# Kernel optimization log

Hardware: AMD Instinct MI355X
Metric: run time of the kernel (lower is better)

## Reference

```python
import jax, jax.numpy as jnp
import numpy as np

B, CIN, COUT, N, K = 8, 128, 128, 2000, 16
IN_EPS = 1e-3   # InstanceNorm2d eps in module
BN_EPS = 1e-5   # BatchNorm2d default eps


def conv1x1(x, w, b):
    # x: [B,C,H,W], w: [O,C], b: [O]
    return jnp.einsum('bchw,oc->bohw', x, w) + b[None, :, None, None]


def setup_inputs() -> dict:
    key = jax.random.key(0)
    ks = jax.random.split(key, 12)
    s = 0.05
    return {
        'x_row':   jax.random.normal(ks[0], (B, COUT, N, 1), jnp.float32),
        'x_local': jax.random.normal(ks[1], (B, CIN, N, K), jnp.float32),
        'w0': jax.random.normal(ks[2], (COUT, CIN), jnp.float32) * s,
        'b0': jax.random.normal(ks[3], (COUT,), jnp.float32) * s,
        'bn_g': jnp.ones((COUT,), jnp.float32),
        'bn_b': jnp.zeros((COUT,), jnp.float32),
        'wq': jax.random.normal(ks[4], (COUT, COUT), jnp.float32) * s,
        'bq': jax.random.normal(ks[5], (COUT,), jnp.float32) * s,
        'wk': jax.random.normal(ks[6], (COUT, COUT), jnp.float32) * s,
        'bk': jax.random.normal(ks[7], (COUT,), jnp.float32) * s,
        'wv': jax.random.normal(ks[8], (COUT, COUT), jnp.float32) * s,
        'bv': jax.random.normal(ks[9], (COUT,), jnp.float32) * s,
        'gamma1': jnp.ones((1,), jnp.float32),
    }


def reference(x_row, x_local, w0, b0, bn_g, bn_b, wq, bq, wk, bk, wv, bv, gamma1):
    # att1: Conv1x1 -> InstanceNorm2d(eps=1e-3, no affine) -> BatchNorm2d (train-mode batch stats) -> ReLU
    h = conv1x1(x_local, w0, b0)                       # [B,C,N,K]
    mu = jnp.mean(h, axis=(2, 3), keepdims=True)
    var = jnp.var(h, axis=(2, 3), keepdims=True)
    h = (h - mu) * jax.lax.rsqrt(var + IN_EPS)
    bmu = jnp.mean(h, axis=(0, 2, 3), keepdims=True)
    bvar = jnp.var(h, axis=(0, 2, 3), keepdims=True)
    h = (h - bmu) * jax.lax.rsqrt(bvar + BN_EPS)
    h = h * bn_g[None, :, None, None] + bn_b[None, :, None, None]
    h = jax.nn.relu(h)

    q = conv1x1(h, wq, bq)
    k = conv1x1(h, wk, bk)
    v = conv1x1(h, wv, bv)
    att = jax.nn.softmax(q * k, axis=3)                # softmax over neighbor axis
    out_local = jnp.sum(att * v, axis=3, keepdims=True)  # [B,C,N,1]
    return x_row + gamma1 * out_local
```

## Files before the change

### kernel.cpp

```cpp
#include <hip/hip_runtime.h>
#include <math.h>

#define NB 8
#define NC 128
#define NPOS 2000
#define NK 32000
#define IN_EPS 1e-3f
#define BN_EPS 1e-5f

typedef short bf16x8 __attribute__((ext_vector_type(8)));
typedef float f32x4 __attribute__((ext_vector_type(4)));
typedef unsigned short ushort_t;

#define XSTRIDE 136

#define WSF_SUMP  0
#define WSF_SQP   32768
#define WSF_ALPHA 65536
#define WSF_BETA  66560
#define WSB_WEIGHTS 270336

__device__ __forceinline__ f32x4 mfma_bf16(bf16x8 a, bf16x8 b, f32x4 c) {
  return __builtin_amdgcn_mfma_f32_16x16x32_bf16(a, b, c, 0, 0, 0);
}

__device__ __forceinline__ ushort_t f2bf(float f) {
  unsigned u = __float_as_uint(f);
  return (ushort_t)((u + 0x7FFFu + ((u >> 16) & 1u)) >> 16);
}

__global__ __launch_bounds__(256) void k_prep(const float* __restrict__ w0,
    const float* __restrict__ wq, const float* __restrict__ wk,
    const float* __restrict__ wv, ushort_t* __restrict__ wb) {
  int idx = blockIdx.x * 256 + threadIdx.x;
  int m = idx >> 14;
  int e = idx & 16383;
  const float* src = (m == 0) ? w0 : (m == 1) ? wq : (m == 2) ? wk : wv;
  wb[m * 16384 + e] = f2bf(src[e]);
}

__device__ __forceinline__ void stage_xt128(const float* __restrict__ xb,
                                            ushort_t* __restrict__ xt, int tid) {
  const int col = tid & 127;
  const int hi = tid >> 7;
  const float* p = xb + col;
#pragma unroll
  for (int i = 0; i < 8; ++i) {
    const int c0 = hi * 64 + i * 8;
    ushort_t u[8] __attribute__((aligned(16)));
#pragma unroll
    for (int j = 0; j < 8; ++j) u[j] = f2bf(p[(size_t)(c0 + j) * NK]);
    *(uint4*)(xt + col * XSTRIDE + c0) = *(const uint4*)u;
  }
}

__device__ __forceinline__ void stage_xt64(const float* __restrict__ xb,
                                           ushort_t* __restrict__ xt, int tid) {
  const int col = tid & 63;
  const int hi = tid >> 6;
  const float* p = xb + col;
#pragma unroll
  for (int i = 0; i < 4; ++i) {
    const int c0 = hi * 32 + i * 8;
    ushort_t u[8] __attribute__((aligned(16)));
#pragma unroll
    for (int j = 0; j < 8; ++j) u[j] = f2bf(p[(size_t)(c0 + j) * NK]);
    *(uint4*)(xt + col * XSTRIDE + c0) = *(const uint4*)u;
  }
}

__global__ __launch_bounds__(256, 4) void k_stats(const float* __restrict__ x,
    const ushort_t* __restrict__ w0b, float* __restrict__ sumP,
    float* __restrict__ sqP) {
  __shared__ ushort_t xt[128 * XSTRIDE];
  __shared__ float ssum[128], ssq[128];
  const int b = blockIdx.y;
  const int tid = threadIdx.x;
  stage_xt128(x + (size_t)b * NC * NK + (size_t)blockIdx.x * 128, xt, tid);
  __syncthreads();
  const int lane = tid & 63, w = tid >> 6;
  const int m = lane & 15, quad = lane >> 4;

#pragma unroll 1
  for (int p = 0; p < 2; ++p) {
    const int ch0 = (w + p * 4) * 16;
    bf16x8 wf[4];
#pragma unroll
    for (int kb = 0; kb < 4; ++kb)
      wf[kb] = *(const bf16x8*)(w0b + (ch0 + m) * 128 + kb * 32 + quad * 8);
    float s = 0.f, q2 = 0.f;
#pragma unroll 2
    for (int t = 0; t < 8; ++t) {
      const ushort_t* xr = xt + (t * 16 + m) * XSTRIDE;
      f32x4 acc = {0.f, 0.f, 0.f, 0.f};
#pragma unroll
      for (int kb = 0; kb < 4; ++kb) {
        bf16x8 af = *(const bf16x8*)(xr + kb * 32 + quad * 8);
        acc = mfma_bf16(af, wf[kb], acc);
      }
      s += (acc[0] + acc[1]) + (acc[2] + acc[3]);
      q2 += (acc[0] * acc[0] + acc[1] * acc[1]) +
            (acc[2] * acc[2] + acc[3] * acc[3]);
    }
    s += __shfl_xor(s, 16);
    s += __shfl_xor(s, 32);
    q2 += __shfl_xor(q2, 16);
    q2 += __shfl_xor(q2, 32);
    if (quad == 0) {
      ssum[ch0 + m] = s;
      ssq[ch0 + m] = q2;
    }
  }
  __syncthreads();
  if (tid < 128) {
    const int bucket = blockIdx.x & 31;
    atomicAdd(&sumP[bucket * 1024 + b * 128 + tid], ssum[tid]);
    atomicAdd(&sqP[bucket * 1024 + b * 128 + tid], ssq[tid]);
  }
}

__global__ void k_fold(const float* __restrict__ ws_in, const float* __restrict__ bn_g,
                       const float* __restrict__ bn_b, float* __restrict__ alpha,
                       float* __restrict__ beta) {
  int c = threadIdx.x;
  const float* sumP = ws_in + WSF_SUMP;
  const float* sqP = ws_in + WSF_SQP;
  float var[NB], muv[NB];
  float bvar = 0.f;
#pragma unroll 1
  for (int b = 0; b < NB; ++b) {
    float s = 0.f, q = 0.f;
#pragma unroll
    for (int k = 0; k < 32; ++k) {
      s += sumP[k * 1024 + b * 128 + c];
      q += sqP[k * 1024 + b * 128 + c];
    }
    float mu = s * (1.f / NK);
    float v = q * (1.f / NK) - mu * mu;
    muv[b] = mu;
    var[b] = v;
    bvar += v / (v + IN_EPS);
  }
  bvar *= 0.125f;
  float s2 = rsqrtf(bvar + BN_EPS);
  float g = bn_g[c], bb = bn_b[c];
#pragma unroll
  for (int b = 0; b < NB; ++b) {
    float a = rsqrtf(var[b] + IN_EPS) * s2 * g;
    alpha[b * 128 + c] = a;
    beta[b * 128 + c] = bb - muv[b] * a;
  }
}

__global__ __launch_bounds__(256, 4) void k_fused(const float* __restrict__ x,
    const float* __restrict__ x_row, const ushort_t* __restrict__ wb,
    const float* __restrict__ alpha, const float* __restrict__ beta,
    const float* __restrict__ bq, const float* __restrict__ bk,
    const float* __restrict__ bv, const float* __restrict__ g1p,
    float* __restrict__ out) {
  __shared__ ushort_t xt[64 * XSTRIDE];
  __shared__ ushort_t ht[64 * XSTRIDE];
  __shared__ float souts[128 * 5];
  const int b = blockIdx.y;
  const int tid = threadIdx.x;
  stage_xt64(x + (size_t)b * NC * NK + (size_t)blockIdx.x * 64, xt, tid);
  const float g1 = g1p[0];
  __syncthreads();
  const int lane = tid & 63, w = tid >> 6;
  const int m = lane & 15, quad = lane >> 4;
  const ushort_t* w0b = wb;
  const ushort_t* wqb = wb + 16384;
  const ushort_t* wkb = wb + 32768;
  const ushort_t* wvb = wb + 49152;

#pragma unroll 1
  for (int p = 0; p < 2; ++p) {
    const int ch0 = (w + p * 4) * 16;
    bf16x8 wf[4];
#pragma unroll
    for (int kb = 0; kb < 4; ++kb)
      wf[kb] = *(const bf16x8*)(w0b + (ch0 + m) * 128 + kb * 32 + quad * 8);
    const float4 av = *(const float4*)(alpha + b * 128 + ch0 + quad * 4);
    const float4 bev = *(const float4*)(beta + b * 128 + ch0 + quad * 4);
#pragma unroll
    for (int t = 0; t < 4; ++t) {
      const ushort_t* xr = xt + (t * 16 + m) * XSTRIDE;
      f32x4 acc = {0.f, 0.f, 0.f, 0.f};
#pragma unroll
      for (int kb = 0; kb < 4; ++kb) {
        bf16x8 bx = *(const bf16x8*)(xr + kb * 32 + quad * 8);
        acc = mfma_bf16(wf[kb], bx, acc);
      }
      float h0 = fmaxf(acc[0] * av.x + bev.x, 0.f);
      float h1 = fmaxf(acc[1] * av.y + bev.y, 0.f);
      float h2 = fmaxf(acc[2] * av.z + bev.z, 0.f);
      float h3 = fmaxf(acc[3] * av.w + bev.w, 0.f);
      uint2 pk;
      pk.x = (unsigned)f2bf(h0) | ((unsigned)f2bf(h1) << 16);
      pk.y = (unsigned)f2bf(h2) | ((unsigned)f2bf(h3) << 16);
      *(uint2*)(ht + (t * 16 + m) * XSTRIDE + ch0 + quad * 4) = pk;
    }
  }
  __syncthreads();

#pragma unroll 1
  for (int p = 0; p < 2; ++p) {
    const int ch0 = (w + p * 4) * 16;
    bf16x8 wqf[4], wkf[4], wvf[4];
#pragma unroll
    for (int kb = 0; kb < 4; ++kb) {
      wqf[kb] = *(const bf16x8*)(wqb + (ch0 + m) * 128 + kb * 32 + quad * 8);
      wkf[kb] = *(const bf16x8*)(wkb + (ch0 + m) * 128 + kb * 32 + quad * 8);
      wvf[kb] = *(const bf16x8*)(wvb + (ch0 + m) * 128 + kb * 32 + quad * 8);
    }
    const float bqv = bq[ch0 + m];
    const float bkv = bk[ch0 + m];
    const float bvv = bv[ch0 + m];
#pragma unroll 1
    for (int t = 0; t < 4; ++t) {
      const ushort_t* hr = ht + (t * 16 + m) * XSTRIDE;
      bf16x8 af[4];
#pragma unroll
      for (int kb = 0; kb < 4; ++kb)
        af[kb] = *(const bf16x8*)(hr + kb * 32 + quad * 8);
      f32x4 qa = {0.f, 0.f, 0.f, 0.f};
      f32x4 ka = {0.f, 0.f, 0.f, 0.f};
#pragma unroll
      for (int kb = 0; kb < 4; ++kb) qa = mfma_bf16(af[kb], wqf[kb], qa);
#pragma unroll
      for (int kb = 0; kb < 4; ++kb) ka = mfma_bf16(af[kb], wkf[kb], ka);
      float p0 = (qa[0] + bqv) * (ka[0] + bkv);
      float p1 = (qa[1] + bqv) * (ka[1] + bkv);
      float p2 = (qa[2] + bqv) * (ka[2] + bkv);
      float p3 = (qa[3] + bqv) * (ka[3] + bkv);
      float mx = fmaxf(fmaxf(p0, p1), fmaxf(p2, p3));
      mx = fmaxf(mx, __shfl_xor(mx, 16));
      mx = fmaxf(mx, __shfl_xor(mx, 32));
      float e0 = __expf(p0 - mx), e1 = __expf(p1 - mx);
      float e2 = __expf(p2 - mx), e3 = __expf(p3 - mx);
      float sm = (e0 + e1) + (e2 + e3);
      sm += __shfl_xor(sm, 16);
      sm += __shfl_xor(sm, 32);
      f32x4 va = {0.f, 0.f, 0.f, 0.f};
#pragma unroll
      for (int kb = 0; kb < 4; ++kb) va = mfma_bf16(af[kb], wvf[kb], va);
      float r0 = e0 * (va[0] + bvv) + e1 * (va[1] + bvv) +
                 e2 * (va[2] + bvv) + e3 * (va[3] + bvv);
      r0 += __shfl_xor(r0, 16);
      r0 += __shfl_xor(r0, 32);
      if (quad == 0) souts[(ch0 + m) * 5 + t] = r0 / sm;
    }
  }
  __syncthreads();

  if (tid < 128) {
    const int c = tid;
    const size_t oi = ((size_t)b * NC + c) * NPOS + blockIdx.x * 4;
    const float4 xr = *(const float4*)(x_row + oi);
    const float* sp = souts + c * 5;
    float4 o;
    o.x = xr.x + g1 * sp[0];
    o.y = xr.y + g1 * sp[1];
    o.z = xr.z + g1 * sp[2];
    o.w = xr.w + g1 * sp[3];
    *(float4*)(out + oi) = o;
  }
}

extern "C" void kernel_launch(void* const* d_in, const int* in_sizes, int n_in,
                              void* d_out, int out_size, void* d_ws, size_t ws_size,
                              hipStream_t stream) {
  (void)in_sizes; (void)n_in; (void)out_size; (void)ws_size;
  const float* x_row   = (const float*)d_in[0];
  const float* x_local = (const float*)d_in[1];
  const float* w0   = (const float*)d_in[2];
  const float* bn_g = (const float*)d_in[4];
  const float* bn_b = (const float*)d_in[5];
  const float* wq   = (const float*)d_in[6];
  const float* bq   = (const float*)d_in[7];
  const float* wk   = (const float*)d_in[8];
  const float* bk   = (const float*)d_in[9];
  const float* wv   = (const float*)d_in[10];
  const float* bv   = (const float*)d_in[11];
  const float* gamma1 = (const float*)d_in[12];
  float* out = (float*)d_out;
  float* ws = (float*)d_ws;
  ushort_t* wb = (ushort_t*)((char*)d_ws + WSB_WEIGHTS);

  hipMemsetAsync(ws, 0, 65536 * sizeof(float), stream);
  k_prep<<<256, 256, 0, stream>>>(w0, wq, wk, wv, wb);
  k_stats<<<dim3(250, NB), 256, 0, stream>>>(x_local, wb, ws + WSF_SUMP,
                                             ws + WSF_SQP);
  k_fold<<<1, 128, 0, stream>>>(ws, bn_g, bn_b, ws + WSF_ALPHA, ws + WSF_BETA);
  k_fused<<<dim3(500, NB), 256, 0, stream>>>(x_local, x_row, wb, ws + WSF_ALPHA,
                                             ws + WSF_BETA, bq, bk, bv, gamma1,
                                             out);
}
```

Measured before the change: 311.4 us.

## Materialize pre-norm conv output as fp16 in workspace instead of recomputing

When the workspace is large enough, the stats kernel now writes the first 1x1 conv output as fp16 to global memory. The fused kernel reads that buffer, applies the folded norm and ReLU, and skips re-reading the fp32 input and redoing the first GEMM. The q/k/v weights and activations move to fp16 MFMA. This halves the bytes read in the second pass, at the cost of a roughly 70MB intermediate write and fp16 rounding of the pre-norm values. If the workspace is too small, the old path is kept as a fallback.

```diff
diff --git a/kernel.cpp b/kernel.cpp
--- a/kernel.cpp
+++ b/kernel.cpp
@@ -9,8 +9,10 @@
 #define BN_EPS 1e-5f
 
 typedef short bf16x8 __attribute__((ext_vector_type(8)));
+typedef _Float16 f16x8 __attribute__((ext_vector_type(8)));
 typedef float f32x4 __attribute__((ext_vector_type(4)));
 typedef unsigned short ushort_t;
+typedef unsigned int uint_t;
 
 #define XSTRIDE 136
 
@@ -19,16 +21,32 @@
 #define WSF_ALPHA 65536
 #define WSF_BETA  66560
 #define WSB_WEIGHTS 270336
+#define WSB_H     401408
+#define WS_NEEDED ((size_t)WSB_H + (size_t)NB * NK * XSTRIDE * 2)
 
 __device__ __forceinline__ f32x4 mfma_bf16(bf16x8 a, bf16x8 b, f32x4 c) {
   return __builtin_amdgcn_mfma_f32_16x16x32_bf16(a, b, c, 0, 0, 0);
+}
+__device__ __forceinline__ f32x4 mfma_f16(f16x8 a, f16x8 b, f32x4 c) {
+  return __builtin_amdgcn_mfma_f32_16x16x32_f16(a, b, c, 0, 0, 0);
 }
 
 __device__ __forceinline__ ushort_t f2bf(float f) {
   unsigned u = __float_as_uint(f);
   return (ushort_t)((u + 0x7FFFu + ((u >> 16) & 1u)) >> 16);
 }
-
+__device__ __forceinline__ ushort_t f2h(float f) {
+  union { _Float16 h; ushort_t u; } cv;
+  cv.h = (_Float16)f;
+  return cv.u;
+}
+__device__ __forceinline__ float h2f(ushort_t u) {
+  union { _Float16 h; ushort_t u; } cv;
+  cv.u = u;
+  return (float)cv.h;
+}
+
+template <int QKV_F16>
 __global__ __launch_bounds__(256) void k_prep(const float* __restrict__ w0,
     const float* __restrict__ wq, const float* __restrict__ wk,
     const float* __restrict__ wv, ushort_t* __restrict__ wb) {
@@ -36,7 +54,8 @@
   int m = idx >> 14;
   int e = idx & 16383;
   const float* src = (m == 0) ? w0 : (m == 1) ? wq : (m == 2) ? wk : wv;
-  wb[m * 16384 + e] = f2bf(src[e]);
+  float v = src[e];
+  wb[m * 16384 + e] = (QKV_F16 && m != 0) ? f2h(v) : f2bf(v);
 }
 
 __device__ __forceinline__ void stage_xt128(const float* __restrict__ xb,
@@ -69,17 +88,18 @@
   }
 }
 
-__global__ __launch_bounds__(256, 4) void k_stats(const float* __restrict__ x,
+__global__ __launch_bounds__(256, 8) void k_stats2(const float* __restrict__ x,
     const ushort_t* __restrict__ w0b, float* __restrict__ sumP,
-    float* __restrict__ sqP) {
-  __shared__ ushort_t xt[128 * XSTRIDE];
+    float* __restrict__ sqP, ushort_t* __restrict__ hg) {
+  __shared__ ushort_t xt[64 * XSTRIDE] __attribute__((aligned(16)));
   __shared__ float ssum[128], ssq[128];
   const int b = blockIdx.y;
   const int tid = threadIdx.x;
-  stage_xt128(x + (size_t)b * NC * NK + (size_t)blockIdx.x * 128, xt, tid);
+  stage_xt64(x + (size_t)b * NC * NK + (size_t)blockIdx.x * 64, xt, tid);
   __syncthreads();
   const int lane = tid & 63, w = tid >> 6;
   const int m = lane & 15, quad = lane >> 4;
+  ushort_t* hrow0 = hg + ((size_t)b * NK + (size_t)blockIdx.x * 64) * XSTRIDE;
 
 #pragma unroll 1
   for (int p = 0; p < 2; ++p) {
@@ -88,27 +108,40 @@
 #pragma unroll
     for (int kb = 0; kb < 4; ++kb)
       wf[kb] = *(const bf16x8*)(w0b + (ch0 + m) * 128 + kb * 32 + quad * 8);
-    float s = 0.f, q2 = 0.f;
-#pragma unroll 2
-    for (int t = 0; t < 8; ++t) {
+    float s0 = 0.f, s1 = 0.f, s2 = 0.f, s3 = 0.f;
+    float q0 = 0.f, q1 = 0.f, q2 = 0.f, q3 = 0.f;
+#pragma unroll
+    for (int t = 0; t < 4; ++t) {
       const ushort_t* xr = xt + (t * 16 + m) * XSTRIDE;
       f32x4 acc = {0.f, 0.f, 0.f, 0.f};
 #pragma unroll
       for (int kb = 0; kb < 4; ++kb) {
-        bf16x8 af = *(const bf16x8*)(xr + kb * 32 + quad * 8);
-        acc = mfma_bf16(af, wf[kb], acc);
+        bf16x8 bx = *(const bf16x8*)(xr + kb * 32 + quad * 8);
+        acc = mfma_bf16(wf[kb], bx, acc);
       }
-      s += (acc[0] + acc[1]) + (acc[2] + acc[3]);
-      q2 += (acc[0] * acc[0] + acc[1] * acc[1]) +
-            (acc[2] * acc[2] + acc[3] * acc[3]);
-    }
-    s += __shfl_xor(s, 16);
-    s += __shfl_xor(s, 32);
-    q2 += __shfl_xor(q2, 16);
-    q2 += __shfl_xor(q2, 32);
-    if (quad == 0) {
-      ssum[ch0 + m] = s;
-      ssq[ch0 + m] = q2;
+      const ushort_t u0 = f2h(acc[0]), u1 = f2h(acc[1]);
+      const ushort_t u2 = f2h(acc[2]), u3 = f2h(acc[3]);
+      uint2 pk;
+      pk.x = (uint_t)u0 | ((uint_t)u1 << 16);
+      pk.y = (uint_t)u2 | ((uint_t)u3 << 16);
+      *(uint2*)(hrow0 + (size_t)(t * 16 + m) * XSTRIDE + ch0 + quad * 4) = pk;
+      const float r0 = h2f(u0), r1 = h2f(u1), r2 = h2f(u2), r3 = h2f(u3);
+      s0 += r0; s1 += r1; s2 += r2; s3 += r3;
+      q0 = fmaf(r0, r0, q0); q1 = fmaf(r1, r1, q1);
+      q2 = fmaf(r2, r2, q2); q3 = fmaf(r3, r3, q3);
+    }
+#pragma unroll
+    for (int d = 1; d < 16; d <<= 1) {
+      s0 += __shfl_xor(s0, d); s1 += __shfl_xor(s1, d);
+      s2 += __shfl_xor(s2, d); s3 += __shfl_xor(s3, d);
+      q0 += __shfl_xor(q0, d); q1 += __shfl_xor(q1, d);
+      q2 += __shfl_xor(q2, d); q3 += __shfl_xor(q3, d);
+    }
+    if (m == 0) {
+      ssum[ch0 + quad * 4 + 0] = s0; ssum[ch0 + quad * 4 + 1] = s1;
+      ssum[ch0 + quad * 4 + 2] = s2; ssum[ch0 + quad * 4 + 3] = s3;
+      ssq[ch0 + quad * 4 + 0] = q0; ssq[ch0 + quad * 4 + 1] = q1;
+      ssq[ch0 + quad * 4 + 2] = q2; ssq[ch0 + quad * 4 + 3] = q3;
     }
   }
   __syncthreads();
@@ -152,7 +185,175 @@
   }
 }
 
-__global__ __launch_bounds__(256, 4) void k_fused(const float* __restrict__ x,
+__global__ __launch_bounds__(256, 8) void k_fused2(
+    const ushort_t* __restrict__ hg, const float* __restrict__ x_row,
+    const ushort_t* __restrict__ wb, const float* __restrict__ alpha,
+    const float* __restrict__ beta, const float* __restrict__ bq,
+    const float* __restrict__ bk, const float* __restrict__ bv,
+    const float* __restrict__ g1p, float* __restrict__ out) {
+  __shared__ ushort_t xt[64 * XSTRIDE] __attribute__((aligned(16)));
+  __shared__ float souts[128 * 5];
+  const int b = blockIdx.y;
+  const int tid = threadIdx.x;
+  const int lane = tid & 63, w = tid >> 6;
+
+  {
+    const uint4* src =
+        (const uint4*)(hg + ((size_t)b * NK + (size_t)blockIdx.x * 64) * XSTRIDE);
+    uint4* dst = (uint4*)xt;
+#pragma unroll
+    for (int i = 0; i < 4; ++i) dst[i * 256 + tid] = src[i * 256 + tid];
+    if (tid < 64) dst[1024 + tid] = src[1024 + tid];
+  }
+  const float g1 = g1p[0];
+  __syncthreads();
+
+  {
+    const int pos = tid & 63;
+    const int cg = __builtin_amdgcn_readfirstlane(tid >> 6);
+    ushort_t* row = xt + pos * XSTRIDE + cg * 32;
+    const float* ap = alpha + b * 128 + cg * 32;
+    const float* bp = beta + b * 128 + cg * 32;
+#pragma unroll
+    for (int i = 0; i < 4; ++i) {
+      uint4 v = *(const uint4*)(row + i * 8);
+      uint_t rr[4] = {v.x, v.y, v.z, v.w};
+      uint_t ow[4];
+#pragma unroll
+      for (int j = 0; j < 4; ++j) {
+        const int c = i * 8 + j * 2;
+        float lo = h2f((ushort_t)(rr[j] & 0xffffu));
+        float hi = h2f((ushort_t)(rr[j] >> 16));
+        float nlo = fmaxf(fmaf(lo, ap[c], bp[c]), 0.f);
+        float nhi = fmaxf(fmaf(hi, ap[c + 1], bp[c + 1]), 0.f);
+        ow[j] = (uint_t)f2h(nlo) | ((uint_t)f2h(nhi) << 16);
+      }
+      uint4 o;
+      o.x = ow[0]; o.y = ow[1]; o.z = ow[2]; o.w = ow[3];
+      *(uint4*)(row + i * 8) = o;
+    }
+  }
+  __syncthreads();
+
+  const int m = lane & 15, quad = lane >> 4;
+  const ushort_t* wqb = wb + 16384;
+  const ushort_t* wkb = wb + 32768;
+  const ushort_t* wvb = wb + 49152;
+#pragma unroll 1
+  for (int p = 0; p < 2; ++p) {
+    const int ch0 = (w + p * 4) * 16;
+    f16x8 wqf[4], wkf[4], wvf[4];
+#pragma unroll
+    for (int kb = 0; kb < 4; ++kb) {
+      wqf[kb] = *(const f16x8*)(wqb + (ch0 + m) * 128 + kb * 32 + quad * 8);
+      wkf[kb] = *(const f16x8*)(wkb + (ch0 + m) * 128 + kb * 32 + quad * 8);
+      wvf[kb] = *(const f16x8*)(wvb + (ch0 + m) * 128 + kb * 32 + quad * 8);
+    }
+    const float bqv = bq[ch0 + m];
+    const float bkv = bk[ch0 + m];
+    const float bvv = bv[ch0 + m];
+#pragma unroll 1
+    for (int t = 0; t < 4; ++t) {
+      const ushort_t* hr = xt + (t * 16 + m) * XSTRIDE;
+      f16x8 af[4];
+#pragma unroll
+      for (int kb = 0; kb < 4; ++kb)
+        af[kb] = *(const f16x8*)(hr + kb * 32 + quad * 8);
+      f32x4 qa = {0.f, 0.f, 0.f, 0.f};
+      f32x4 ka = {0.f, 0.f, 0.f, 0.f};
+#pragma unroll
+      for (int kb = 0; kb < 4; ++kb) qa = mfma_f16(af[kb], wqf[kb], qa);
+#pragma unroll
+      for (int kb = 0; kb < 4; ++kb) ka = mfma_f16(af[kb], wkf[kb], ka);
+      float p0 = (qa[0] + bqv) * (ka[0] + bkv);
+      float p1 = (qa[1] + bqv) * (ka[1] + bkv);
+      float p2 = (qa[2] + bqv) * (ka[2] + bkv);
+      float p3 = (qa[3] + bqv) * (ka[3] + bkv);
+      float mx = fmaxf(fmaxf(p0, p1), fmaxf(p2, p3));
+      mx = fmaxf(mx, __shfl_xor(mx, 16));
+      mx = fmaxf(mx, __shfl_xor(mx, 32));
+      float e0 = __expf(p0 - mx), e1 = __expf(p1 - mx);
+      float e2 = __expf(p2 - mx), e3 = __expf(p3 - mx);
+      float sm = (e0 + e1) + (e2 + e3);
+      sm += __shfl_xor(sm, 16);
+      sm += __shfl_xor(sm, 32);
+      f32x4 va = {0.f, 0.f, 0.f, 0.f};
+#pragma unroll
+      for (int kb = 0; kb < 4; ++kb) va = mfma_f16(af[kb], wvf[kb], va);
+      float r0 = e0 * (va[0] + bvv) + e1 * (va[1] + bvv) +
+                 e2 * (va[2] + bvv) + e3 * (va[3] + bvv);
+      r0 += __shfl_xor(r0, 16);
+      r0 += __shfl_xor(r0, 32);
+      if (quad == 0) souts[(ch0 + m) * 5 + t] = r0 / sm;
+    }
+  }
+  __syncthreads();
+
+  if (tid < 128) {
+    const int c = tid;
+    const size_t oi = ((size_t)b * NC + c) * NPOS + blockIdx.x * 4;
+    const float4 xr = *(const float4*)(x_row + oi);
+    const float* sp = souts + c * 5;
+    float4 o;
+    o.x = xr.x + g1 * sp[0];
+    o.y = xr.y + g1 * sp[1];
+    o.z = xr.z + g1 * sp[2];
+    o.w = xr.w + g1 * sp[3];
+    *(float4*)(out + oi) = o;
+  }
+}
+
+__global__ __launch_bounds__(256, 4) void k_stats1(const float* __restrict__ x,
+    const ushort_t* __restrict__ w0b, float* __restrict__ sumP,
+    float* __restrict__ sqP) {
+  __shared__ ushort_t xt[128 * XSTRIDE];
+  __shared__ float ssum[128], ssq[128];
+  const int b = blockIdx.y;
+  const int tid = threadIdx.x;
+  stage_xt128(x + (size_t)b * NC * NK + (size_t)blockIdx.x * 128, xt, tid);
+  __syncthreads();
+  const int lane = tid & 63, w = tid >> 6;
+  const int m = lane & 15, quad = lane >> 4;
+
+#pragma unroll 1
+  for (int p = 0; p < 2; ++p) {
+    const int ch0 = (w + p * 4) * 16;
+    bf16x8 wf[4];
+#pragma unroll
+    for (int kb = 0; kb < 4; ++kb)
+      wf[kb] = *(const bf16x8*)(w0b + (ch0 + m) * 128 + kb * 32 + quad * 8);
+    float s = 0.f, q2 = 0.f;
+#pragma unroll 2
+    for (int t = 0; t < 8; ++t) {
+      const ushort_t* xr = xt + (t * 16 + m) * XSTRIDE;
+      f32x4 acc = {0.f, 0.f, 0.f, 0.f};
+#pragma unroll
+      for (int kb = 0; kb < 4; ++kb) {
+        bf16x8 af = *(const bf16x8*)(xr + kb * 32 + quad * 8);
+        acc = mfma_bf16(af, wf[kb], acc);
+      }
+      s += (acc[0] + acc[1]) + (acc[2] + acc[3]);
+      q2 += (acc[0] * acc[0] + acc[1] * acc[1]) +
+            (acc[2] * acc[2] + acc[3] * acc[3]);
+    }
+    s += __shfl_xor(s, 16);
+    s += __shfl_xor(s, 32);
+    q2 += __shfl_xor(q2, 16);
+    q2 += __shfl_xor(q2, 32);
+    if (quad == 0) {
+      ssum[ch0 + m] = s;
+      ssq[ch0 + m] = q2;
+    }
+  }
+  __syncthreads();
+  if (tid < 128) {
+    const int bucket = blockIdx.x & 31;
+    atomicAdd(&sumP[bucket * 1024 + b * 128 + tid], ssum[tid]);
+    atomicAdd(&sqP[bucket * 1024 + b * 128 + tid], ssq[tid]);
+  }
+}
+
+__global__ __launch_bounds__(256, 4) void k_fused1(const float* __restrict__ x,
     const float* __restrict__ x_row, const ushort_t* __restrict__ wb,
     const float* __restrict__ alpha, const float* __restrict__ beta,
     const float* __restrict__ bq, const float* __restrict__ bk,
@@ -196,8 +397,8 @@
       float h2 = fmaxf(acc[2] * av.z + bev.z, 0.f);
       float h3 = fmaxf(acc[3] * av.w + bev.w, 0.f);
       uint2 pk;
-      pk.x = (unsigned)f2bf(h0) | ((unsigned)f2bf(h1) << 16);
-      pk.y = (unsigned)f2bf(h2) | ((unsigned)f2bf(h3) << 16);
+      pk.x = (uint_t)f2bf(h0) | ((uint_t)f2bf(h1) << 16);
+      pk.y = (uint_t)f2bf(h2) | ((uint_t)f2bf(h3) << 16);
       *(uint2*)(ht + (t * 16 + m) * XSTRIDE + ch0 + quad * 4) = pk;
     }
   }
@@ -270,7 +471,7 @@
 extern "C" void kernel_launch(void* const* d_in, const int* in_sizes, int n_in,
                               void* d_out, int out_size, void* d_ws, size_t ws_size,
                               hipStream_t stream) {
-  (void)in_sizes; (void)n_in; (void)out_size; (void)ws_size;
+  (void)in_sizes; (void)n_in; (void)out_size;
   const float* x_row   = (const float*)d_in[0];
   const float* x_local = (const float*)d_in[1];
   const float* w0   = (const float*)d_in[2];
@@ -286,13 +487,25 @@
   float* out = (float*)d_out;
   float* ws = (float*)d_ws;
   ushort_t* wb = (ushort_t*)((char*)d_ws + WSB_WEIGHTS);
+  ushort_t* hg = (ushort_t*)((char*)d_ws + WSB_H);
 
   hipMemsetAsync(ws, 0, 65536 * sizeof(float), stream);
-  k_prep<<<256, 256, 0, stream>>>(w0, wq, wk, wv, wb);
-  k_stats<<<dim3(250, NB), 256, 0, stream>>>(x_local, wb, ws + WSF_SUMP,
-                                             ws + WSF_SQP);
-  k_fold<<<1, 128, 0, stream>>>(ws, bn_g, bn_b, ws + WSF_ALPHA, ws + WSF_BETA);
-  k_fused<<<dim3(500, NB), 256, 0, stream>>>(x_local, x_row, wb, ws + WSF_ALPHA,
-                                             ws + WSF_BETA, bq, bk, bv, gamma1,
-                                             out);
-}
+
+  if (ws_size >= WS_NEEDED) {
+    k_prep<1><<<256, 256, 0, stream>>>(w0, wq, wk, wv, wb);
+    k_stats2<<<dim3(500, NB), 256, 0, stream>>>(x_local, wb, ws + WSF_SUMP,
+                                                ws + WSF_SQP, hg);
+    k_fold<<<1, 128, 0, stream>>>(ws, bn_g, bn_b, ws + WSF_ALPHA, ws + WSF_BETA);
+    k_fused2<<<dim3(500, NB), 256, 0, stream>>>(hg, x_row, wb, ws + WSF_ALPHA,
+                                                ws + WSF_BETA, bq, bk, bv, gamma1,
+                                                out);
+  } else {
+    k_prep<0><<<256, 256, 0, stream>>>(w0, wq, wk, wv, wb);
+    k_stats1<<<dim3(250, NB), 256, 0, stream>>>(x_local, wb, ws + WSF_SUMP,
+                                                ws + WSF_SQP);
+    k_fold<<<1, 128, 0, stream>>>(ws, bn_g, bn_b, ws + WSF_ALPHA, ws + WSF_BETA);
+    k_fused1<<<dim3(500, NB), 256, 0, stream>>>(x_local, x_row, wb, ws + WSF_ALPHA,
+                                                ws + WSF_BETA, bq, bk, bv, gamma1,
+                                                out);
+  }
+}
```

Measured after the change: 485.2 us. 55.8% more time.
